# Optimization experiments

Measured on AMD Instinct MI355X. Metric: run time of the kernel, lower is better.

Reference implementation:

```python
import jax, jax.numpy as jnp
import numpy as np

B, T, LIE, OBS = 8, 2048, 32, 64
D = 2 * LIE  # d_head


def setup_inputs() -> dict:
    key = jax.random.key(0)
    ks = jax.random.split(key, 12)
    positions = jax.random.normal(ks[0], (B, T, D, D), dtype=jnp.float32)
    content_emb = jax.random.normal(ks[1], (B, T, OBS), dtype=jnp.float32)
    F = jnp.eye(LIE, dtype=jnp.float32) + 0.01 * jax.random.normal(ks[2], (LIE, LIE), dtype=jnp.float32)
    log_Q_diag = 0.1 * jax.random.normal(ks[3], (LIE,), dtype=jnp.float32)
    log_R_diag = 0.1 * jax.random.normal(ks[4], (OBS,), dtype=jnp.float32)
    H_w = jax.random.normal(ks[5], (OBS, LIE), dtype=jnp.float32) * (1.0 / np.sqrt(LIE))
    det_w1 = jax.random.normal(ks[6], (64, OBS), dtype=jnp.float32) * (1.0 / np.sqrt(OBS))
    det_b1 = jnp.zeros((64,), dtype=jnp.float32)
    det_w2 = jax.random.normal(ks[7], (1, 64), dtype=jnp.float32) * (1.0 / 8.0)
    det_b2 = jnp.zeros((1,), dtype=jnp.float32)
    obs_w = jax.random.normal(ks[8], (OBS, OBS), dtype=jnp.float32) * (1.0 / np.sqrt(OBS))
    obs_b = jnp.zeros((OBS,), dtype=jnp.float32)
    return {"positions": positions, "content_emb": content_emb, "F": F,
            "log_Q_diag": log_Q_diag, "log_R_diag": log_R_diag, "H_w": H_w,
            "det_w1": det_w1, "det_b1": det_b1, "det_w2": det_w2, "det_b2": det_b2,
            "obs_w": obs_w, "obs_b": obs_b}


def reference(positions, content_emb, F, log_Q_diag, log_R_diag, H_w,
              det_w1, det_b1, det_w2, det_b2, obs_w, obs_b):
    Bn, Tn, d, _ = positions.shape
    L = log_Q_diag.shape[0]
    Qd = jnp.exp(log_Q_diag)            # (L,) process noise diag
    Rd = jnp.exp(log_R_diag)            # (O,) measurement noise diag
    # landmark detector MLP + sigmoid (all timesteps at once)
    h = jax.nn.relu(content_emb @ det_w1.T + det_b1)
    probs = jax.nn.sigmoid((h @ det_w2.T + det_b2)[..., 0])   # (B,T)
    z_all = content_emb @ obs_w.T + obs_b                      # (B,T,O)
    ar = jnp.arange(L)
    I_L = jnp.eye(L, dtype=positions.dtype)
    Sigma0 = jnp.broadcast_to(I_L * 0.01, (Bn, L, L))

    def step(Sigma, inp):
        pos_t, z_t, prob_t = inp  # (B,d,d), (B,O), (B,)
        # predict: F Sigma F^T + Q
        Sigma = jnp.einsum('ij,bjk,lk->bil', F, Sigma, F) + jnp.diag(Qd)[None]
        # extract diagonal 2x2 blocks -> (B,L,2,2)
        resh = pos_t.reshape(Bn, L, 2, L, 2).transpose(0, 1, 3, 2, 4)  # (B,L,L,2,2)
        blocks = resh[:, ar, ar]
        # log map SO(2): theta = atan2(R10, R00)
        mu = jnp.arctan2(blocks[..., 1, 0], blocks[..., 0, 0])  # (B,L)
        # Kalman update
        S = jnp.einsum('oi,bij,pj->bop', H_w, Sigma, H_w) + jnp.diag(Rd)[None]
        K = jnp.einsum('bij,oj,bop->bip', Sigma, H_w, jnp.linalg.inv(S))  # (B,L,O)
        y = z_t - mu @ H_w.T
        mu_c = mu + jnp.einsum('bio,bo->bi', K, y)
        IKH = I_L[None] - K @ H_w
        Sigma_u = jnp.einsum('bij,bjk,blk->bil', IKH, Sigma, IKH) \
                  + jnp.einsum('bio,o,bjo->bij', K, Rd, K)
        # exp map SO(2)
        c, s = jnp.cos(mu_c), jnp.sin(mu_c)
        nb = jnp.stack([jnp.stack([c, -s], -1), jnp.stack([s, c], -1)], -2)  # (B,L,2,2)
        gate = jnp.any(prob_t > 0.5)  # torch branch: update only if any landmark
        a4 = prob_t[:, None, None, None]
        blended = jnp.where(gate, a4 * nb + (1.0 - a4) * blocks, blocks)
        a3 = prob_t[:, None, None]
        Sigma_out = jnp.where(gate, a3 * Sigma_u + (1.0 - a3) * Sigma, Sigma)
        corr_t = resh.at[:, ar, ar].set(blended).transpose(0, 1, 3, 2, 4).reshape(Bn, d, d)
        return Sigma_out, (corr_t, Sigma_out)

    _, (corr, covs) = jax.lax.scan(
        step, Sigma0,
        (positions.transpose(1, 0, 2, 3), z_all.transpose(1, 0, 2), probs.T))
    return corr.transpose(1, 0, 2, 3), covs.transpose(1, 0, 2, 3), probs
```

## Files before the change

kernel.cpp:

```cpp
#include <hip/hip_runtime.h>
#include <math.h>

#define TT 2048
#define NB 8
#define CH 16
#define BURN 32
#define NCH (TT / CH)
#define WMAX (BURN + CH)
#define NSCAN (NCH * NB)

typedef __attribute__((ext_vector_type(16))) float f32x16;
typedef __attribute__((ext_vector_type(8))) __bf16 bf16x8;

__device__ __forceinline__ bf16x8 ph(const f32x16& x, int base) {
  bf16x8 r;
#pragma unroll
  for (int d = 0; d < 8; ++d) r[d] = (__bf16)x[base + d];
  return r;
}
__device__ __forceinline__ bf16x8 pl(const f32x16& x, int base) {
  bf16x8 r;
#pragma unroll
  for (int d = 0; d < 8; ++d) {
    float t = x[base + d];
    r[d] = (__bf16)(t - (float)((__bf16)t));
  }
  return r;
}
struct FragsH { bf16x8 h0, h1; };
struct Frags { bf16x8 h0, l0, h1, l1; };
__device__ __forceinline__ FragsH mkh(const f32x16& x) { return {ph(x, 0), ph(x, 8)}; }
__device__ __forceinline__ Frags mkf(const f32x16& x) {
  return {ph(x, 0), pl(x, 0), ph(x, 8), pl(x, 8)};
}

#define MFMA_B __builtin_amdgcn_mfma_f32_32x32x16_bf16
__device__ __forceinline__ f32x16 mmA(bf16x8 a0, bf16x8 a1, bf16x8 b0, bf16x8 b1, f32x16 c) {
  c = MFMA_B(a0, b0, c, 0, 0, 0);
  c = MFMA_B(a1, b1, c, 0, 0, 0);
  return c;
}
__device__ __forceinline__ f32x16 mm6(const Frags& A, const Frags& B, f32x16 c) {
  f32x16 u = {};
  c = MFMA_B(A.h0, B.h0, c, 0, 0, 0);  u = MFMA_B(A.h0, B.l0, u, 0, 0, 0);
  c = MFMA_B(A.h1, B.h1, c, 0, 0, 0);  u = MFMA_B(A.h1, B.l1, u, 0, 0, 0);
  c = MFMA_B(A.l0, B.h0, c, 0, 0, 0);  u = MFMA_B(A.l1, B.h1, u, 0, 0, 0);
  return c + u;
}

__global__ __launch_bounds__(256) void k_setup(const float* __restrict__ Hw,
                                               const float* __restrict__ logR,
                                               float* __restrict__ cinv,
                                               float* __restrict__ htr) {
  __shared__ float C[32][33];
  __shared__ float rinv[64];
  int tid = threadIdx.x;
  if (tid < 64) rinv[tid] = expf(-logR[tid]);
  __syncthreads();
  int i = tid >> 3, j0 = (tid & 7) << 2;
  float a0 = 0.f, a1 = 0.f, a2 = 0.f, a3 = 0.f;
  for (int o = 0; o < 64; ++o) {
    float hio = Hw[o * 32 + i] * rinv[o];
    a0 += hio * Hw[o * 32 + j0];
    a1 += hio * Hw[o * 32 + j0 + 1];
    a2 += hio * Hw[o * 32 + j0 + 2];
    a3 += hio * Hw[o * 32 + j0 + 3];
  }
  C[i][j0] = a0; C[i][j0 + 1] = a1; C[i][j0 + 2] = a2; C[i][j0 + 3] = a3;
  for (int e = 0; e < 8; ++e) {
    int idx = tid * 8 + e;
    int ii = idx >> 6, o = idx & 63;
    htr[idx] = Hw[o * 32 + ii] * rinv[o];
  }
  __syncthreads();
  for (int k = 0; k < 32; ++k) {
    float ip = 1.0f / C[k][k];
    __syncthreads();
    if (tid < 32 && tid != k) C[k][tid] = -C[k][tid] * ip;
    __syncthreads();
    if (i != k) {
      float f = C[i][k];
      for (int q = 0; q < 4; ++q) {
        int j = j0 + q;
        if (j != k) C[i][j] += f * C[k][j];
      }
    }
    __syncthreads();
    if (tid < 32) {
      if (tid == k) C[k][k] = ip; else C[tid][k] *= ip;
    }
    __syncthreads();
  }
  cinv[i * 32 + j0]     = C[i][j0];
  cinv[i * 32 + j0 + 1] = C[i][j0 + 1];
  cinv[i * 32 + j0 + 2] = C[i][j0 + 2];
  cinv[i * 32 + j0 + 3] = C[i][j0 + 3];
}

__global__ __launch_bounds__(256) void k_obs(const float* __restrict__ emb,
                                             const float* __restrict__ w1,
                                             const float* __restrict__ b1,
                                             const float* __restrict__ w2,
                                             const float* __restrict__ b2,
                                             const float* __restrict__ ow,
                                             const float* __restrict__ ob,
                                             float* __restrict__ probs_out,
                                             float* __restrict__ zws) {
  int wave = threadIdx.x >> 6, lane = threadIdx.x & 63;
  int row = blockIdx.x * 4 + wave;
  float xv = emb[(size_t)row * 64 + lane];
  const float4* w1v = (const float4*)(w1 + lane * 64);
  float hacc = b1[lane];
#pragma unroll
  for (int i4 = 0; i4 < 16; ++i4) {
    float4 wv = w1v[i4];
    hacc += __shfl(xv, i4 * 4, 64) * wv.x + __shfl(xv, i4 * 4 + 1, 64) * wv.y +
            __shfl(xv, i4 * 4 + 2, 64) * wv.z + __shfl(xv, i4 * 4 + 3, 64) * wv.w;
  }
  float h = fmaxf(hacc, 0.f);
  float s = h * w2[lane];
#pragma unroll
  for (int off = 32; off; off >>= 1) s += __shfl_xor(s, off, 64);
  float prob = 1.0f / (1.0f + expf(-(s + b2[0])));
  if (lane == 0) probs_out[row] = prob;
  const float4* owv = (const float4*)(ow + lane * 64);
  float zacc = ob[lane];
#pragma unroll
  for (int i4 = 0; i4 < 16; ++i4) {
    float4 wv = owv[i4];
    zacc += __shfl(xv, i4 * 4, 64) * wv.x + __shfl(xv, i4 * 4 + 1, 64) * wv.y +
            __shfl(xv, i4 * 4 + 2, 64) * wv.z + __shfl(xv, i4 * 4 + 3, 64) * wv.w;
  }
  zws[(size_t)row * 64 + lane] = zacc;
}

__global__ void k_gate(const float* __restrict__ probs_out, int* __restrict__ gate) {
  int t = blockIdx.x * 256 + threadIdx.x;
  if (t < TT) {
    int g = 0;
    for (int b = 0; b < NB; ++b) g |= (probs_out[b * TT + t] > 0.5f) ? 1 : 0;
    gate[t] = g;
  }
}

__global__ __launch_bounds__(64, 1) void k_scan_copy(const float* __restrict__ Fg,
                                                     const float* __restrict__ logQ,
                                                     const float* __restrict__ probs_out,
                                                     const int* __restrict__ gate,
                                                     const float* __restrict__ cinv,
                                                     float* __restrict__ covs,
                                                     float* __restrict__ su_ws,
                                                     const float* __restrict__ pos,
                                                     float* __restrict__ corr) {
  const int bid = blockIdx.x;
  const int l = threadIdx.x;

  if (bid >= NSCAN) {
    const int idx = bid - NSCAN;
    const float4* src = (const float4*)(pos + (((size_t)idx) << 12));
    float4* dst = (float4*)(corr + (((size_t)idx) << 12));
#pragma unroll
    for (int k = 0; k < 16; ++k) {
      dst[k * 64 + l] = src[k * 64 + l];
    }
    return;
  }

  __shared__ float probL[WMAX];
  __shared__ int gateL[WMAX];
  const int ck = bid & (NCH - 1), b = bid >> 7;
  const int hh = l >> 5, c = l & 31;
  const int t0 = ck * CH;
  const int beg = (t0 - BURN > 0) ? (t0 - BURN) : 0;
  const int cnt = t0 + CH - beg;

  for (int i = l; i < cnt / 4; i += 64) {
    ((float4*)probL)[i] = ((const float4*)(probs_out + (size_t)b * TT + beg))[i];
    ((int4*)gateL)[i] = ((const int4*)(gate + beg))[i];
  }

  f32x16 vA, vC, vI;
#pragma unroll
  for (int s = 0; s < 2; ++s)
#pragma unroll
    for (int i = 0; i < 8; ++i) {
      int col = 16 * s + 4 * hh + (i & 3) + 8 * (i >> 2);
      int q = i + 8 * s;
      vA[q] = Fg[c * 32 + col] - ((col == c) ? 1.0f : 0.0f);
      vC[q] = cinv[c * 32 + col];
      vI[q] = (col == c) ? 1.0f : 0.0f;
    }
  const FragsH aFh = mkh(vA);
  const FragsH aFl = {pl(vA, 0), pl(vA, 8)};
  const Frags Cf = mkf(vC);
  const FragsH Idh = mkh(vI);

  f32x16 dq, qdv, ciD, sig, Xv;
  float qc = expf(logQ[c]);
#pragma unroll
  for (int q = 0; q < 16; ++q) {
    int rq = (q & 3) + 8 * (q >> 2) + 4 * hh;
    dq[q] = (rq == c) ? 1.0f : 0.0f;
    qdv[q] = (rq == c) ? qc : 0.0f;
    ciD[q] = cinv[rq * 32 + c];
    sig[q] = (rq == c) ? 0.01f : 0.0f;
    Xv[q] = 0.0f;
  }
  bf16x8 Xh0 = ph(Xv, 0), Xh1 = ph(Xv, 8);

  float* cbase = covs + (((size_t)(b * TT + beg)) << 10) + c * 32 + 4 * hh;
  float* sbase = su_ws + (((size_t)(b * TT + beg)) << 10) + c * 32 + 4 * hh;
  __syncthreads();
  float a3 = probL[0];
  int g = gateL[0];

#pragma unroll 1
  for (int tt = 0; tt < cnt; ++tt) {
    const int nn = (tt + 1 < cnt) ? tt + 1 : tt;
    float a3n = probL[nn];
    int gn = gateL[nn];
    const bool wr = (beg + tt >= t0);

    FragsH Sh = mkh(sig);
    f32x16 g2 = mmA(Sh.h0, Sh.h1, aFl.h0, aFl.h1,
                    mmA(Sh.h0, Sh.h1, aFh.h0, aFh.h1, sig));
    FragsH G2h = mkh(g2);
    f32x16 p = mmA(aFl.h0, aFl.h1, G2h.h0, G2h.h1,
                   mmA(aFh.h0, aFh.h1, G2h.h0, G2h.h1, g2 + qdv));

    if (g) {
      const f32x16 zz = {};
      f32x16 M = p + ciD;
      Frags Mf = mkf(M);
      f32x16 T = mmA(Mf.h0, Mf.h1, Xh0, Xh1, zz);
      float csum = 0.f;
#pragma unroll
      for (int q = 0; q < 16; ++q) csum += fabsf(dq[q] - T[q]);
      csum += __shfl_xor(csum, 32);

      if (__all(csum < 0.55f)) {
        FragsH Th = mkh(T);
        f32x16 U = mmA(Xh0, Xh1, Th.h0, Th.h1, zz);
        Xv = 2.0f * Xv - U;
        if (!__all(csum < 0.12f)) {
          FragsH Xn = mkh(Xv);
          f32x16 T2 = mmA(Mf.h0, Mf.h1, Xn.h0, Xn.h1, zz);
          FragsH T2h = mkh(T2);
          f32x16 U2 = mmA(Xn.h0, Xn.h1, T2h.h0, T2h.h1, zz);
          Xv = 2.0f * Xv - U2;
          if (!__all(csum < 0.30f)) {
            FragsH Xn3 = mkh(Xv);
            f32x16 T3n = mmA(Mf.h0, Mf.h1, Xn3.h0, Xn3.h1, zz);
            FragsH T3h = mkh(T3n);
            f32x16 U3 = mmA(Xn3.h0, Xn3.h1, T3h.h0, T3h.h1, zz);
            Xv = 2.0f * Xv - U3;
          }
        }
        FragsH Xp = mkh(Xv);
        f32x16 Xt = mmA(Xp.h0, Xp.h1, Idh.h0, Idh.h1, zz);
        f32x16 Xs = 0.5f * (Xv + Xt);
        Frags Xsf = mkf(Xs);
        f32x16 T3 = mm6(Mf, Xsf, zz);
        f32x16 E3 = dq - T3;
        FragsH E3h = mkh(E3);
        Xv = mmA(Xsf.h0, Xsf.h1, E3h.h0, E3h.h1, Xs);
      } else {
        float m[16];
#pragma unroll
        for (int q = 0; q < 16; ++q) m[q] = M[q];
#pragma unroll
        for (int k = 0; k < 32; ++k) {
          const int hk = (k >> 2) & 1;
          const int qk = (k & 3) | ((k >> 3) << 2);
          float pv = __shfl(m[qk], k + 32 * hk, 64);
          float r0 = __builtin_amdgcn_rcpf(pv);
          float ip = r0 * (2.0f - pv * r0);
          const bool myrow = (c == k);
#pragma unroll
          for (int q = 0; q < 16; ++q) {
            bool isdiag = (q == qk) && (hh == hk);
            float sc = -m[q] * ip;
            m[q] = (myrow && !isdiag) ? sc : m[q];
          }
          float fk = __shfl(m[qk], c + 32 * hk, 64);
          float prv[16];
#pragma unroll
          for (int q = 0; q < 16; ++q) prv[q] = __shfl(m[q], k + 32 * hh, 64);
#pragma unroll
          for (int q = 0; q < 16; ++q) {
            bool pivcol = (q == qk) && (hh == hk);
            float upd = fmaf(fk, prv[q], m[q]);
            m[q] = (!myrow && !pivcol) ? upd : m[q];
          }
          float cf = myrow ? ip : fk * ip;
          m[qk] = (hh == hk) ? cf : m[qk];
        }
#pragma unroll
        for (int q = 0; q < 16; ++q) Xv[q] = m[q];
      }

      const f32x16 zz2 = {};
      Xh0 = ph(Xv, 0);
      Xh1 = ph(Xv, 8);
      Frags Xf = {Xh0, pl(Xv, 0), Xh1, pl(Xv, 8)};
      f32x16 t5 = mm6(Xf, Cf, zz2);
      f32x16 Y = dq - t5;
      Frags Yf = mkf(Y);
      f32x16 Su = mm6(Cf, Yf, zz2);

      const float om = 1.0f - a3;
      f32x16 sg = a3 * Su + om * p;
      sig = sg;
      if (wr) {
#pragma unroll
        for (int j4 = 0; j4 < 4; ++j4) {
          float4 v;
          v.x = sg[4 * j4]; v.y = sg[4 * j4 + 1];
          v.z = sg[4 * j4 + 2]; v.w = sg[4 * j4 + 3];
          *(float4*)(cbase + 8 * j4) = v;
          float4 w;
          w.x = Su[4 * j4]; w.y = Su[4 * j4 + 1];
          w.z = Su[4 * j4 + 2]; w.w = Su[4 * j4 + 3];
          *(float4*)(sbase + 8 * j4) = w;
        }
      }
    } else {
      sig = p;
      if (wr) {
#pragma unroll
        for (int j4 = 0; j4 < 4; ++j4) {
          float4 v;
          v.x = p[4 * j4]; v.y = p[4 * j4 + 1];
          v.z = p[4 * j4 + 2]; v.w = p[4 * j4 + 3];
          *(float4*)(cbase + 8 * j4) = v;
        }
      }
    }
    cbase += 1024;
    sbase += 1024;
    a3 = a3n;
    g = gn;
  }
}

__global__ __launch_bounds__(64) void k_diag(const float* __restrict__ pos,
                                             const float* __restrict__ zws,
                                             const float* __restrict__ probs_out,
                                             const int* __restrict__ gate,
                                             const float* __restrict__ Hw,
                                             const float* __restrict__ htr,
                                             const float* __restrict__ su_ws,
                                             float* __restrict__ corr) {
  const int bid = blockIdx.x;
  const int b = bid >> 11, t = bid & 2047;
  if (!gate[t]) return;
  const size_t pbase = ((size_t)bid) << 12;
  const float* src = pos + pbase;
  float* dst = corr + pbase;
  const int tid = threadIdx.x;
  __shared__ float muL[32], yL[64], vL[32];
  float a4 = probs_out[b * TT + t];
  float p00 = 0.f, p01 = 0.f, p10 = 0.f, p11 = 0.f, mu = 0.f;
  if (tid < 32) {
    int ii = tid;
    p00 = src[(2 * ii) * 64 + 2 * ii];
    p01 = src[(2 * ii) * 64 + 2 * ii + 1];
    p10 = src[(2 * ii + 1) * 64 + 2 * ii];
    p11 = src[(2 * ii + 1) * 64 + 2 * ii + 1];
    mu = atan2f(p10, p00);
    muL[ii] = mu;
  }
  __syncthreads();
  {
    int o = tid;
    float zo = zws[((size_t)bid) * 64 + o];
    const float4* hrow = (const float4*)(Hw + o * 32);
    float s = 0.f;
#pragma unroll
    for (int i4 = 0; i4 < 8; ++i4) {
      float4 hv = hrow[i4];
      s += muL[i4 * 4] * hv.x + muL[i4 * 4 + 1] * hv.y +
           muL[i4 * 4 + 2] * hv.z + muL[i4 * 4 + 3] * hv.w;
    }
    yL[o] = zo - s;
  }
  __syncthreads();
  if (tid < 32) {
    const float4* hr = (const float4*)(htr + tid * 64);
    float s = 0.f;
#pragma unroll
    for (int j4 = 0; j4 < 16; ++j4) {
      float4 hv = hr[j4];
      s += yL[j4 * 4] * hv.x + yL[j4 * 4 + 1] * hv.y +
           yL[j4 * 4 + 2] * hv.z + yL[j4 * 4 + 3] * hv.w;
    }
    vL[tid] = s;
  }
  __syncthreads();
  if (tid < 32) {
    const float4* srow = (const float4*)(su_ws + (((size_t)bid) << 10) + tid * 32);
    float s = 0.f;
#pragma unroll
    for (int j4 = 0; j4 < 8; ++j4) {
      float4 sv = srow[j4];
      s += vL[j4 * 4] * sv.x + vL[j4 * 4 + 1] * sv.y +
           vL[j4 * 4 + 2] * sv.z + vL[j4 * 4 + 3] * sv.w;
    }
    float mc = mu + s;
    float cc = cosf(mc), sn = sinf(mc);
    float om = 1.0f - a4;
    float2 r0, r1;
    r0.x = a4 * cc + om * p00;
    r0.y = a4 * (-sn) + om * p01;
    r1.x = a4 * sn + om * p10;
    r1.y = a4 * cc + om * p11;
    *(float2*)(dst + (2 * tid) * 64 + 2 * tid) = r0;
    *(float2*)(dst + (2 * tid + 1) * 64 + 2 * tid) = r1;
  }
}

extern "C" void kernel_launch(void* const* d_in, const int* in_sizes, int n_in,
                              void* d_out, int out_size, void* d_ws, size_t ws_size,
                              hipStream_t stream) {
  const float* pos  = (const float*)d_in[0];
  const float* emb  = (const float*)d_in[1];
  const float* Fg   = (const float*)d_in[2];
  const float* logQ = (const float*)d_in[3];
  const float* logR = (const float*)d_in[4];
  const float* Hw   = (const float*)d_in[5];
  const float* w1   = (const float*)d_in[6];
  const float* b1   = (const float*)d_in[7];
  const float* w2   = (const float*)d_in[8];
  const float* b2   = (const float*)d_in[9];
  const float* ow   = (const float*)d_in[10];
  const float* ob   = (const float*)d_in[11];

  float* corr  = (float*)d_out;
  float* covs  = corr + 67108864;
  float* probs = corr + 83886080;

  float* ws   = (float*)d_ws;
  float* zws  = ws;
  int*   gate = (int*)(ws + 1048576);
  float* cinv = ws + 1050624;
  float* htr  = ws + 1051648;
  float* su   = ws + 1053696;

  hipLaunchKernelGGL(k_setup, dim3(1), dim3(256), 0, stream, Hw, logR, cinv, htr);
  hipLaunchKernelGGL(k_obs, dim3(4096), dim3(256), 0, stream, emb, w1, b1, w2, b2, ow, ob, probs, zws);
  hipLaunchKernelGGL(k_gate, dim3(8), dim3(256), 0, stream, probs, gate);
  hipLaunchKernelGGL(k_scan_copy, dim3(NSCAN + NB * TT), dim3(64), 0, stream,
                     Fg, logQ, probs, gate, cinv, covs, su, pos, corr);
  hipLaunchKernelGGL(k_diag, dim3(NB * TT), dim3(64), 0, stream,
                     pos, zws, probs, gate, Hw, htr, su, corr);
}
```

Measured before the change: 427.6 us.

## Interleave positions-to-corr copy into scan loop instead of separate copy blocks

Removes the 16384 dedicated copy blocks. Each of the 1024 scan blocks now copies its own 16K-float4 slice of positions into corr, software-pipelined across scan iterations with a 6-float4 register buffer, plus a tail loop for the remainder. This aims to hide the bandwidth-bound copy behind the latency-bound serial scan and to cut block launch overhead. In exchange it adds register pressure and puts memory traffic inside the scan's critical loop, and the copy now runs on only 1024 wavefronts, which may lower achieved bandwidth.

```diff
diff --git a/kernel.cpp b/kernel.cpp
--- a/kernel.cpp
+++ b/kernel.cpp
@@ -152,27 +152,18 @@
                                                      float* __restrict__ su_ws,
                                                      const float* __restrict__ pos,
                                                      float* __restrict__ corr) {
-  const int bid = blockIdx.x;
-  const int l = threadIdx.x;
-
-  if (bid >= NSCAN) {
-    const int idx = bid - NSCAN;
-    const float4* src = (const float4*)(pos + (((size_t)idx) << 12));
-    float4* dst = (float4*)(corr + (((size_t)idx) << 12));
-#pragma unroll
-    for (int k = 0; k < 16; ++k) {
-      dst[k * 64 + l] = src[k * 64 + l];
-    }
-    return;
-  }
-
   __shared__ float probL[WMAX];
   __shared__ int gateL[WMAX];
+  const int bid = blockIdx.x, l = threadIdx.x;
   const int ck = bid & (NCH - 1), b = bid >> 7;
   const int hh = l >> 5, c = l & 31;
   const int t0 = ck * CH;
   const int beg = (t0 - BURN > 0) ? (t0 - BURN) : 0;
   const int cnt = t0 + CH - beg;
+
+  const float4* psrc = (const float4*)pos + (((size_t)bid) << 14);
+  float4* pdst = (float4*)corr + (((size_t)bid) << 14);
+  float4 cb[6];
 
   for (int i = l; i < cnt / 4; i += 64) {
     ((float4*)probL)[i] = ((const float4*)(probs_out + (size_t)b * TT + beg))[i];
@@ -220,6 +211,19 @@
     float a3n = probL[nn];
     int gn = gateL[nn];
     const bool wr = (beg + tt >= t0);
+
+    if (tt > 0) {
+#pragma unroll
+      for (int j = 0; j < 6; ++j) {
+        int kk = (tt - 1) * 6 + j;
+        if (kk < 256) pdst[kk * 64 + l] = cb[j];
+      }
+    }
+#pragma unroll
+    for (int j = 0; j < 6; ++j) {
+      int kk = tt * 6 + j;
+      if (kk < 256) cb[j] = psrc[kk * 64 + l];
+    }
 
     FragsH Sh = mkh(sig);
     f32x16 g2 = mmA(Sh.h0, Sh.h1, aFl.h0, aFl.h1,
@@ -341,6 +345,16 @@
     a3 = a3n;
     g = gn;
   }
+
+  {
+    const int ttl = cnt - 1;
+#pragma unroll
+    for (int j = 0; j < 6; ++j) {
+      int kk = ttl * 6 + j;
+      if (kk < 256) pdst[kk * 64 + l] = cb[j];
+    }
+    for (int kk = cnt * 6; kk < 256; ++kk) pdst[kk * 64 + l] = psrc[kk * 64 + l];
+  }
 }
 
 __global__ __launch_bounds__(64) void k_diag(const float* __restrict__ pos,
@@ -449,7 +463,7 @@
   hipLaunchKernelGGL(k_setup, dim3(1), dim3(256), 0, stream, Hw, logR, cinv, htr);
   hipLaunchKernelGGL(k_obs, dim3(4096), dim3(256), 0, stream, emb, w1, b1, w2, b2, ow, ob, probs, zws);
   hipLaunchKernelGGL(k_gate, dim3(8), dim3(256), 0, stream, probs, gate);
-  hipLaunchKernelGGL(k_scan_copy, dim3(NSCAN + NB * TT), dim3(64), 0, stream,
+  hipLaunchKernelGGL(k_scan_copy, dim3(NSCAN), dim3(64), 0, stream,
                      Fg, logQ, probs, gate, cinv, covs, su, pos, corr);
   hipLaunchKernelGGL(k_diag, dim3(NB * TT), dim3(64), 0, stream,
                      pos, zws, probs, gate, Hw, htr, su, corr);
```

Result: slower. 630.3 us (+47.4%).
